# Optimization experiments

Measured on AMD Instinct MI355X. Metric: run time of the kernel, lower is better.

The kernel has to match this reference:

```python
import jax, jax.numpy as jnp
import numpy as np


def setup_inputs() -> dict:
    key = jax.random.key(0)
    ks = jax.random.split(key, 6)
    L, B, S, D = 2, 32, 2048, 1024
    dec_hidden = jax.random.normal(ks[0], (L, B, D), dtype=jnp.float32)
    enc_out = jax.random.normal(ks[1], (B, S, D), dtype=jnp.float32)
    mask = jax.random.randint(ks[2], (B, S), 0, 2, dtype=jnp.int32)
    sc = 1.0 / np.sqrt(D)
    W_dec = jax.random.normal(ks[3], (D, D), dtype=jnp.float32) * sc
    W_enc = jax.random.normal(ks[4], (D, D), dtype=jnp.float32) * sc
    w_att = jax.random.normal(ks[5], (D, 1), dtype=jnp.float32) * sc
    return {
        "decoder_hidden": dec_hidden,
        "encoder_outputs": enc_out,
        "mask": mask,
        "W_dec": W_dec,
        "b_dec": jnp.zeros((D,), jnp.float32),
        "W_enc": W_enc,
        "b_enc": jnp.zeros((D,), jnp.float32),
        "w_att": w_att,
        "b_att": jnp.zeros((1,), jnp.float32),
    }


def reference(decoder_hidden, encoder_outputs, mask, W_dec, b_dec, W_enc, b_enc, w_att, b_att):
    # decoder_hidden: [L, B, Dd] -> take last layer, project to enc dim: [B, 1, De]
    dec_proj = decoder_hidden[-1] @ W_dec + b_dec            # [B, De]
    enc_proj = jnp.einsum("bse,ef->bsf", encoder_outputs, W_enc) + b_enc  # [B, S, De]
    energy = jnp.tanh(dec_proj[:, None, :] + enc_proj)        # [B, S, De]
    scores = jnp.einsum("bse,eo->bso", energy, w_att)[..., 0] + b_att[0]  # [B, S]
    scores = jnp.where(mask == 0, jnp.float32(-1e10), scores)
    attn = jax.nn.softmax(scores, axis=1)                     # [B, S]
    context = jnp.einsum("bs,bse->be", attn, encoder_outputs)[:, None, :]  # [B, 1, De]
    return context, attn
```

## Files before the change

kernel.cpp:

```cpp
#include <hip/hip_runtime.h>
#include <hip/hip_bf16.h>

constexpr int LAY = 2;
constexpr int BB  = 32;
constexpr int SS  = 2048;
constexpr int DD  = 1024;

typedef unsigned short u16;
typedef short  short8  __attribute__((ext_vector_type(8)));
typedef u16    u16x8   __attribute__((ext_vector_type(8)));
typedef float  floatx4 __attribute__((ext_vector_type(4)));

__device__ inline float bf2f(u16 u) {
    union { unsigned int i; float f; } v; v.i = ((unsigned int)u) << 16; return v.f;
}
__device__ inline u16 f2bf_rn(float f) {
    union { float f; unsigned int i; } v; v.f = f;
    unsigned int x = v.i;
    return (u16)((x + 0x7FFFu + ((x >> 16) & 1u)) >> 16);
}

__device__ __forceinline__ void gload_lds16(const u16* g, u16* l) {
    __builtin_amdgcn_global_load_lds(
        (const __attribute__((address_space(1))) void*)g,
        (__attribute__((address_space(3))) void*)l, 16, 0, 0);
}

__global__ __launch_bounds__(256) void convert_enc(const float* __restrict__ enc,
                                                   u16* __restrict__ encbf) {
    size_t gid = (size_t)blockIdx.x * 256 + threadIdx.x;
    #pragma unroll 4
    for (int it = 0; it < 16; ++it) {
        size_t i = (it * 524288ull + gid) * 8;
        floatx4 v0 = *reinterpret_cast<const floatx4*>(enc + i);
        floatx4 v1 = *reinterpret_cast<const floatx4*>(enc + i + 4);
        u16x8 r;
        #pragma unroll
        for (int j = 0; j < 4; ++j) { r[j] = f2bf_rn(v0[j]); r[4 + j] = f2bf_rn(v1[j]); }
        *reinterpret_cast<u16x8*>(encbf + i) = r;
    }
}

__global__ __launch_bounds__(256) void transpose_wenc(const float* __restrict__ W,
                                                      u16* __restrict__ wT) {
    int gid = blockIdx.x * 256 + threadIdx.x;
    int n = gid & 1023, c = gid >> 10;
    int k0 = c * 8;
    u16x8 r;
    #pragma unroll
    for (int j = 0; j < 8; ++j) r[j] = f2bf_rn(W[(size_t)(k0 + j) * DD + n]);
    *reinterpret_cast<u16x8*>(&wT[(size_t)n * DD + k0]) = r;
}

__global__ __launch_bounds__(256) void dec_proj_kernel(
    const float* __restrict__ dec_hidden, const float* __restrict__ W_dec,
    const float* __restrict__ b_dec, float* __restrict__ dec_proj) {
    int kc = blockIdx.x, cb = blockIdx.y, b = blockIdx.z, t = threadIdx.x;
    int col = cb * 256 + t;
    const float* h = dec_hidden + (LAY - 1) * BB * DD + b * DD + kc * 256;
    const float* Wp = W_dec + (size_t)kc * 256 * DD + col;
    float a0 = 0.f, a1 = 0.f, a2 = 0.f, a3 = 0.f;
    for (int e = 0; e < 256; e += 4) {
        a0 += h[e + 0] * Wp[(size_t)(e + 0) * DD];
        a1 += h[e + 1] * Wp[(size_t)(e + 1) * DD];
        a2 += h[e + 2] * Wp[(size_t)(e + 2) * DD];
        a3 += h[e + 3] * Wp[(size_t)(e + 3) * DD];
    }
    float v = (a0 + a1) + (a2 + a3);
    if (kc == 0) v += b_dec[col];
    atomicAdd(&dec_proj[b * DD + col], v);
}

__global__ __launch_bounds__(256) void score_gemm_bf(
    const u16* __restrict__ enc,
    const u16* __restrict__ wT,
    const float* __restrict__ dec_proj,
    const float* __restrict__ b_enc, const float* __restrict__ w_att,
    float* __restrict__ scores) {
    __shared__ u16 As[128 * 64];
    __shared__ u16 Bs[128 * 64];

    const int tid  = threadIdx.x;
    const int bn   = blockIdx.x;
    const int bm   = blockIdx.y;
    const int row0 = bm * 128, col0 = bn * 128;
    const int lane = tid & 63, w = tid >> 6;
    const int wm   = w >> 1,  wn = w & 1;
    const int quad = lane >> 4, l16 = lane & 15;

    const int srow = w * 8 + (lane >> 3);
    const int scol = (((lane & 7) ^ (lane >> 3)) * 8);

    floatx4 acc[4][4];
    #pragma unroll
    for (int i = 0; i < 4; ++i)
        #pragma unroll
        for (int j = 0; j < 4; ++j)
            acc[i][j] = (floatx4){0.f, 0.f, 0.f, 0.f};

    for (int kt = 0; kt < DD / 64; ++kt) {
        const int k0 = kt * 64;
        __syncthreads();
        #pragma unroll
        for (int i = 0; i < 4; ++i) {
            gload_lds16(&enc[(size_t)(row0 + i * 32 + srow) * DD + k0 + scol],
                        &As[(i * 32 + w * 8) * 64]);
            gload_lds16(&wT [(size_t)(col0 + i * 32 + srow) * DD + k0 + scol],
                        &Bs[(i * 32 + w * 8) * 64]);
        }
        __syncthreads();
        #pragma unroll
        for (int ks = 0; ks < 2; ++ks) {
            short8 a[4], b[4];
            #pragma unroll
            for (int tm = 0; tm < 4; ++tm) {
                int r = wm * 64 + tm * 16 + l16;
                int kcs = (ks * 4 + quad) ^ (l16 & 7);
                a[tm] = *reinterpret_cast<const short8*>(&As[r * 64 + kcs * 8]);
            }
            #pragma unroll
            for (int tn = 0; tn < 4; ++tn) {
                int r = wn * 64 + tn * 16 + l16;
                int kcs = (ks * 4 + quad) ^ (l16 & 7);
                b[tn] = *reinterpret_cast<const short8*>(&Bs[r * 64 + kcs * 8]);
            }
            #pragma unroll
            for (int tm = 0; tm < 4; ++tm)
                #pragma unroll
                for (int tn = 0; tn < 4; ++tn)
                    acc[tm][tn] = __builtin_amdgcn_mfma_f32_16x16x32_bf16(
                        a[tm], b[tn], acc[tm][tn], 0, 0, 0);
        }
    }

    const int bIdx = row0 / SS;
    const float* dp = dec_proj + bIdx * DD;
    float cvec[4], wvv[4];
    #pragma unroll
    for (int tn = 0; tn < 4; ++tn) {
        int n = col0 + wn * 64 + tn * 16 + l16;
        cvec[tn] = dp[n] + b_enc[n];
        wvv[tn]  = w_att[n];
    }
    #pragma unroll
    for (int tm = 0; tm < 4; ++tm) {
        float rs0 = 0.f, rs1 = 0.f, rs2 = 0.f, rs3 = 0.f;
        #pragma unroll
        for (int tn = 0; tn < 4; ++tn) {
            rs0 += tanhf(acc[tm][tn][0] + cvec[tn]) * wvv[tn];
            rs1 += tanhf(acc[tm][tn][1] + cvec[tn]) * wvv[tn];
            rs2 += tanhf(acc[tm][tn][2] + cvec[tn]) * wvv[tn];
            rs3 += tanhf(acc[tm][tn][3] + cvec[tn]) * wvv[tn];
        }
        #pragma unroll
        for (int off = 1; off < 16; off <<= 1) {
            rs0 += __shfl_xor(rs0, off, 64);
            rs1 += __shfl_xor(rs1, off, 64);
            rs2 += __shfl_xor(rs2, off, 64);
            rs3 += __shfl_xor(rs3, off, 64);
        }
        if (l16 == 0) {
            int rbase = row0 + wm * 64 + tm * 16 + quad * 4;
            atomicAdd(&scores[rbase + 0], rs0);
            atomicAdd(&scores[rbase + 1], rs1);
            atomicAdd(&scores[rbase + 2], rs2);
            atomicAdd(&scores[rbase + 3], rs3);
        }
    }
}

__global__ __launch_bounds__(256) void softmax_kernel(
    const float* __restrict__ scores, const int* __restrict__ mask,
    float* __restrict__ attn_out) {
    int b = blockIdx.x, t = threadIdx.x;
    const float* srow = scores + b * SS;
    const int*   mrow = mask + b * SS;
    float vals[8];
    float vmax = -1e30f;
    #pragma unroll
    for (int i = 0; i < 8; ++i) {
        int s = i * 256 + t;
        float v = (mrow[s] == 0) ? -1e10f : srow[s];
        vals[i] = v;
        vmax = fmaxf(vmax, v);
    }
    #pragma unroll
    for (int off = 32; off >= 1; off >>= 1) vmax = fmaxf(vmax, __shfl_xor(vmax, off, 64));
    __shared__ float sm[4];
    if ((t & 63) == 0) sm[t >> 6] = vmax;
    __syncthreads();
    vmax = fmaxf(fmaxf(sm[0], sm[1]), fmaxf(sm[2], sm[3]));
    float sum = 0.f;
    #pragma unroll
    for (int i = 0; i < 8; ++i) { vals[i] = __expf(vals[i] - vmax); sum += vals[i]; }
    #pragma unroll
    for (int off = 32; off >= 1; off >>= 1) sum += __shfl_xor(sum, off, 64);
    __shared__ float ssum[4];
    if ((t & 63) == 0) ssum[t >> 6] = sum;
    __syncthreads();
    sum = ssum[0] + ssum[1] + ssum[2] + ssum[3];
    float inv = 1.f / sum;
    #pragma unroll
    for (int i = 0; i < 8; ++i) attn_out[b * SS + i * 256 + t] = vals[i] * inv;
}

__global__ __launch_bounds__(256) void context_bf(
    const float* __restrict__ attn, const u16* __restrict__ encbf,
    float* __restrict__ ctx) {
    int scb = blockIdx.x;
    int b   = blockIdx.y;
    int d = threadIdx.x * 4;
    const u16*  base = encbf + ((size_t)b * SS + scb * 256) * DD + d;
    const float* ar  = attn + b * SS + scb * 256;
    float a0 = 0.f, a1 = 0.f, a2 = 0.f, a3 = 0.f;
    #pragma unroll 4
    for (int s = 0; s < 256; ++s) {
        u16x8 dummy; (void)dummy;
        unsigned long long v = *reinterpret_cast<const unsigned long long*>(base + (size_t)s * DD);
        float w = ar[s];
        a0 += w * bf2f((u16)(v       & 0xFFFF));
        a1 += w * bf2f((u16)((v >> 16) & 0xFFFF));
        a2 += w * bf2f((u16)((v >> 32) & 0xFFFF));
        a3 += w * bf2f((u16)((v >> 48) & 0xFFFF));
    }
    atomicAdd(&ctx[b * DD + d + 0], a0);
    atomicAdd(&ctx[b * DD + d + 1], a1);
    atomicAdd(&ctx[b * DD + d + 2], a2);
    atomicAdd(&ctx[b * DD + d + 3], a3);
}

extern "C" void kernel_launch(void* const* d_in, const int* in_sizes, int n_in,
                              void* d_out, int out_size, void* d_ws, size_t ws_size,
                              hipStream_t stream) {
    const float* dec_hidden = (const float*)d_in[0];
    const float* enc        = (const float*)d_in[1];
    const int*   mask       = (const int*)d_in[2];
    const float* W_dec      = (const float*)d_in[3];
    const float* b_dec      = (const float*)d_in[4];
    const float* W_enc      = (const float*)d_in[5];
    const float* b_enc      = (const float*)d_in[6];
    const float* w_att      = (const float*)d_in[7];

    float* out = (float*)d_out;
    float* ws  = (float*)d_ws;
    float* dec_proj = ws;
    float* scores   = ws + 32768;
    u16*   wT       = (u16*)(ws + 98304);
    u16*   encbf    = (u16*)(ws + 622592);
    float* attn     = out + 32768;

    hipMemsetAsync(ws, 0, 98304 * sizeof(float), stream);
    hipMemsetAsync(out, 0, 32768 * sizeof(float), stream);

    convert_enc<<<2048, 256, 0, stream>>>(enc, encbf);
    transpose_wenc<<<512, 256, 0, stream>>>(W_enc, wT);
    dec_proj_kernel<<<dim3(4, 4, 32), 256, 0, stream>>>(dec_hidden, W_dec, b_dec, dec_proj);
    score_gemm_bf<<<dim3(8, 512), 256, 0, stream>>>(encbf, wT, dec_proj, b_enc, w_att, scores);
    softmax_kernel<<<32, 256, 0, stream>>>(scores, mask, attn);
    context_bf<<<dim3(8, 32), 256, 0, stream>>>(attn, encbf, out);
}
```

Measured before the change: 692.2 us.

## Use fast tanh, swizzle GEMM block order, widen context loads

```diff
diff --git a/kernel.cpp b/kernel.cpp
--- a/kernel.cpp
+++ b/kernel.cpp
@@ -18,6 +18,11 @@
     union { float f; unsigned int i; } v; v.f = f;
     unsigned int x = v.i;
     return (u16)((x + 0x7FFFu + ((x >> 16) & 1u)) >> 16);
+}
+
+__device__ __forceinline__ float fast_tanh(float x) {
+    float e = __expf(x + x);
+    return 1.0f - 2.0f * __builtin_amdgcn_rcpf(e + 1.0f);
 }
 
 __device__ __forceinline__ void gload_lds16(const u16* g, u16* l) {
@@ -81,8 +86,10 @@
     __shared__ u16 Bs[128 * 64];
 
     const int tid  = threadIdx.x;
-    const int bn   = blockIdx.x;
-    const int bm   = blockIdx.y;
+    const int f    = blockIdx.x;
+    const int swz  = ((f & 7) << 9) | (f >> 3);
+    const int bm   = swz >> 3;
+    const int bn   = swz & 7;
     const int row0 = bm * 128, col0 = bn * 128;
     const int lane = tid & 63, w = tid >> 6;
     const int wm   = w >> 1,  wn = w & 1;
@@ -147,10 +154,10 @@
         float rs0 = 0.f, rs1 = 0.f, rs2 = 0.f, rs3 = 0.f;
         #pragma unroll
         for (int tn = 0; tn < 4; ++tn) {
-            rs0 += tanhf(acc[tm][tn][0] + cvec[tn]) * wvv[tn];
-            rs1 += tanhf(acc[tm][tn][1] + cvec[tn]) * wvv[tn];
-            rs2 += tanhf(acc[tm][tn][2] + cvec[tn]) * wvv[tn];
-            rs3 += tanhf(acc[tm][tn][3] + cvec[tn]) * wvv[tn];
+            rs0 += fast_tanh(acc[tm][tn][0] + cvec[tn]) * wvv[tn];
+            rs1 += fast_tanh(acc[tm][tn][1] + cvec[tn]) * wvv[tn];
+            rs2 += fast_tanh(acc[tm][tn][2] + cvec[tn]) * wvv[tn];
+            rs3 += fast_tanh(acc[tm][tn][3] + cvec[tn]) * wvv[tn];
         }
         #pragma unroll
         for (int off = 1; off < 16; off <<= 1) {
@@ -209,24 +216,24 @@
     float* __restrict__ ctx) {
     int scb = blockIdx.x;
     int b   = blockIdx.y;
-    int d = threadIdx.x * 4;
-    const u16*  base = encbf + ((size_t)b * SS + scb * 256) * DD + d;
-    const float* ar  = attn + b * SS + scb * 256;
-    float a0 = 0.f, a1 = 0.f, a2 = 0.f, a3 = 0.f;
+    int t   = threadIdx.x;
+    int d   = (t & 127) * 8;
+    int sh  = t >> 7;
+    const float* ar  = attn + b * SS + scb * 128;
+    const u16*  base = encbf + ((size_t)b * SS + scb * 128) * DD + d;
+    float a[8];
+    #pragma unroll
+    for (int j = 0; j < 8; ++j) a[j] = 0.f;
     #pragma unroll 4
-    for (int s = 0; s < 256; ++s) {
-        u16x8 dummy; (void)dummy;
-        unsigned long long v = *reinterpret_cast<const unsigned long long*>(base + (size_t)s * DD);
+    for (int so = 0; so < 128; so += 2) {
+        int s = so + sh;
+        u16x8 v = *reinterpret_cast<const u16x8*>(base + (size_t)s * DD);
         float w = ar[s];
-        a0 += w * bf2f((u16)(v       & 0xFFFF));
-        a1 += w * bf2f((u16)((v >> 16) & 0xFFFF));
-        a2 += w * bf2f((u16)((v >> 32) & 0xFFFF));
-        a3 += w * bf2f((u16)((v >> 48) & 0xFFFF));
-    }
-    atomicAdd(&ctx[b * DD + d + 0], a0);
-    atomicAdd(&ctx[b * DD + d + 1], a1);
-    atomicAdd(&ctx[b * DD + d + 2], a2);
-    atomicAdd(&ctx[b * DD + d + 3], a3);
+        #pragma unroll
+        for (int j = 0; j < 8; ++j) a[j] += w * bf2f(v[j]);
+    }
+    #pragma unroll
+    for (int j = 0; j < 8; ++j) atomicAdd(&ctx[b * DD + d + j], a[j]);
 }
 
 extern "C" void kernel_launch(void* const* d_in, const int* in_sizes, int n_in,
@@ -255,7 +262,7 @@
     convert_enc<<<2048, 256, 0, stream>>>(enc, encbf);
     transpose_wenc<<<512, 256, 0, stream>>>(W_enc, wT);
     dec_proj_kernel<<<dim3(4, 4, 32), 256, 0, stream>>>(dec_hidden, W_dec, b_dec, dec_proj);
-    score_gemm_bf<<<dim3(8, 512), 256, 0, stream>>>(encbf, wT, dec_proj, b_enc, w_att, scores);
+    score_gemm_bf<<<4096, 256, 0, stream>>>(encbf, wT, dec_proj, b_enc, w_att, scores);
     softmax_kernel<<<32, 256, 0, stream>>>(scores, mask, attn);
-    context_bf<<<dim3(8, 32), 256, 0, stream>>>(attn, encbf, out);
-}
+    context_bf<<<dim3(16, 32), 256, 0, stream>>>(attn, encbf, out);
+}
```

Measured after the change: 697.8 us. No clear change (+0.8%).
